# Kernel optimization log

Measured on AMD Instinct MI355X. Metric: run time of the kernel, lower is better.

Reference implementation:

```python
import jax, jax.numpy as jnp
import numpy as np

EMBED = 1024
HEADS = 16
HEAD_DIM = EMBED // HEADS
RANK = 8
ALPHA = 16.0
SCALING = ALPHA / RANK  # 2.0
B, T = 2, 2048


def setup_inputs() -> dict:
    key = jax.random.key(0)
    ks = jax.random.split(key, 12)
    d = {
        'x': jax.random.normal(ks[0], (B, T, EMBED), dtype=jnp.float32),
        'Wq': jax.random.normal(ks[1], (EMBED, EMBED), dtype=jnp.float32),
        'Aq': jax.random.normal(ks[2], (EMBED, RANK), dtype=jnp.float32) * 0.01,
        'Bq': jnp.zeros((RANK, EMBED), dtype=jnp.float32),
        'Wk': jax.random.normal(ks[3], (EMBED, EMBED), dtype=jnp.float32),
        'Ak': jax.random.normal(ks[4], (EMBED, RANK), dtype=jnp.float32) * 0.01,
        'Bk': jnp.zeros((RANK, EMBED), dtype=jnp.float32),
        'Wv': jax.random.normal(ks[5], (EMBED, EMBED), dtype=jnp.float32),
        'Av': jax.random.normal(ks[6], (EMBED, RANK), dtype=jnp.float32) * 0.01,
        'Bv': jnp.zeros((RANK, EMBED), dtype=jnp.float32),
        'Wo': jax.random.normal(ks[7], (EMBED, EMBED), dtype=jnp.float32) * (1.0 / np.sqrt(EMBED)),
        'bo': jnp.zeros((EMBED,), dtype=jnp.float32),
    }
    return d


def _lora_linear(x, W, A, Bm):
    # torch F.linear(x, W) == x @ W.T ; LoRA bypass: x @ A @ B * scaling
    base = jnp.einsum('btc,oc->bto', x, W)
    lora = (x @ A) @ Bm * SCALING
    return base + lora


def reference(x, Wq, Aq, Bq, Wk, Ak, Bk, Wv, Av, Bv, Wo, bo):
    b, t, c = x.shape
    q = _lora_linear(x, Wq, Aq, Bq).reshape(b, t, HEADS, HEAD_DIM).transpose(0, 2, 1, 3)
    k = _lora_linear(x, Wk, Ak, Bk).reshape(b, t, HEADS, HEAD_DIM).transpose(0, 2, 1, 3)
    v = _lora_linear(x, Wv, Av, Bv).reshape(b, t, HEADS, HEAD_DIM).transpose(0, 2, 1, 3)
    scores = jnp.einsum('bhqd,bhkd->bhqk', q, k) / np.sqrt(HEAD_DIM).astype(np.float32)
    attn = jax.nn.softmax(scores, axis=-1)
    ctx = jnp.einsum('bhqk,bhkd->bhqd', attn, v)  # [B,H,T,D]
    out = ctx.transpose(0, 2, 1, 3).reshape(b, t, c)
    return jnp.einsum('btc,oc->bto', out, Wo) + bo
```

## Files before the change

### kernel.cpp

```cpp
#include <hip/hip_runtime.h>
#include <hip/hip_bf16.h>
#include <math.h>

#define EMBED 1024
#define HEADS 16
#define HDIM 64
#define RANK 8
#define BB 2
#define TT 2048
#define MTOT (BB*TT)
#define BH (BB*HEADS)

typedef __attribute__((ext_vector_type(8))) short bf16x8;
typedef __attribute__((ext_vector_type(4))) float f32x4;
typedef unsigned short u16;

__device__ __forceinline__ u16 f2bf(float f){
  unsigned u = __float_as_uint(f);
  u += 0x7FFF + ((u >> 16) & 1);
  return (u16)(u >> 16);
}
__device__ __forceinline__ float bf2f(u16 h){ return __uint_as_float(((unsigned)h) << 16); }

__device__ __forceinline__ void stage16(const void* g, void* l){
  __builtin_amdgcn_global_load_lds((const __attribute__((address_space(1))) unsigned int*)g,
                                   (__attribute__((address_space(3))) unsigned int*)l, 16, 0, 0);
}

__global__ void split_x_kernel(const float* __restrict__ x, u16* __restrict__ xhi, u16* __restrict__ xlo){
  int i = blockIdx.x * 256 + threadIdx.x;
  float v = x[i];
  u16 h = f2bf(v);
  xhi[i] = h;
  xlo[i] = f2bf(v - bf2f(h));
}

__global__ void weff_split_kernel(const float* __restrict__ W, const float* __restrict__ A,
                                  const float* __restrict__ Bm,
                                  u16* __restrict__ whi, u16* __restrict__ wlo){
  int i = blockIdx.x * 256 + threadIdx.x;
  int o = i >> 10, c = i & 1023;
  float s = 0.f;
#pragma unroll
  for (int r = 0; r < RANK; ++r) s += A[c*RANK+r] * Bm[r*EMBED+o];
  float v = W[i] + 2.0f * s;
  u16 h = f2bf(v);
  whi[i] = h;
  wlo[i] = f2bf(v - bf2f(h));
}

__global__ void bf16_cast_kernel(const float* __restrict__ W, u16* __restrict__ wb){
  int i = blockIdx.x * 256 + threadIdx.x;
  wb[i] = f2bf(W[i]);
}

__device__ __forceinline__ int swz4(int row){ return (row ^ (row >> 2)) & 3; }

__global__ __launch_bounds__(256)
void qkv_gemm(const u16* __restrict__ Ahi, const u16* __restrict__ Alo,
              const u16* __restrict__ Bhi, const u16* __restrict__ Blo,
              u16* __restrict__ qhi, u16* __restrict__ qlo,
              u16* __restrict__ khi, u16* __restrict__ klo,
              u16* __restrict__ vt)
{
  __shared__ __align__(16) u16 Ah[128*32], Bh[128*32], Al[128*32], Bl[128*32];
  const int t = threadIdx.x, lane = t & 63, w = t >> 6;
  const int wr = w >> 1, wc = w & 1;
  const int fr = lane & 15, fk = lane >> 4;
  const int m0 = blockIdx.y * 128, n0 = blockIdx.x * 128;
  const bool full = (n0 < 2048);

  f32x4 acc[4][4];
#pragma unroll
  for (int i = 0; i < 4; ++i)
#pragma unroll
    for (int j = 0; j < 4; ++j) acc[i][j] = (f32x4){0.f,0.f,0.f,0.f};

  for (int k0 = 0; k0 < EMBED; k0 += 32){
    __syncthreads();
#pragma unroll
    for (int cc = 0; cc < 2; ++cc){
      int cb = w*128 + cc*64;
      int chunk = cb + lane;
      int row = chunk >> 2, slot = chunk & 3;
      int sl = slot ^ swz4(row);
      stage16(Ahi + (size_t)(m0+row)*EMBED + k0 + sl*8, Ah + cb*8);
      stage16(Bhi + (size_t)(n0+row)*EMBED + k0 + sl*8, Bh + cb*8);
      if (full){
        stage16(Alo + (size_t)(m0+row)*EMBED + k0 + sl*8, Al + cb*8);
        stage16(Blo + (size_t)(n0+row)*EMBED + k0 + sl*8, Bl + cb*8);
      }
    }
    __syncthreads();

    bf16x8 ah[4], bh[4], al[4], bl[4];
#pragma unroll
    for (int i = 0; i < 4; ++i){
      int ra = wr*64 + i*16 + fr;
      int oa = ra*32 + (fk ^ swz4(ra))*8;
      ah[i] = *(const bf16x8*)&Ah[oa];
      if (full) al[i] = *(const bf16x8*)&Al[oa];
      int rb = wc*64 + i*16 + fr;
      int ob = rb*32 + (fk ^ swz4(rb))*8;
      bh[i] = *(const bf16x8*)&Bh[ob];
      if (full) bl[i] = *(const bf16x8*)&Bl[ob];
    }
#pragma unroll
    for (int i = 0; i < 4; ++i)
#pragma unroll
      for (int j = 0; j < 4; ++j){
        acc[i][j] = __builtin_amdgcn_mfma_f32_16x16x32_bf16(ah[i], bh[j], acc[i][j], 0,0,0);
        if (full){
          acc[i][j] = __builtin_amdgcn_mfma_f32_16x16x32_bf16(ah[i], bl[j], acc[i][j], 0,0,0);
          acc[i][j] = __builtin_amdgcn_mfma_f32_16x16x32_bf16(al[i], bh[j], acc[i][j], 0,0,0);
        }
      }
  }

  const int mat = (n0 + wc*64) >> 10;
#pragma unroll
  for (int i = 0; i < 4; ++i)
#pragma unroll
    for (int j = 0; j < 4; ++j)
#pragma unroll
      for (int r = 0; r < 4; ++r){
        int gm = m0 + wr*64 + i*16 + fk*4 + r;
        int gn = n0 + wc*64 + j*16 + fr;
        int col = gn & 1023;
        float v = acc[i][j][r];
        int b = gm >> 11, tt2 = gm & 2047, h = col >> 6, d = col & 63;
        if (mat == 2){
          vt[((size_t)(b*HEADS + h)*HDIM + d)*TT + tt2] = f2bf(v);
        } else {
          if (mat == 0) v *= 0.125f;
          size_t idx = ((size_t)(b*HEADS + h)*TT + tt2)*HDIM + d;
          u16 hi = f2bf(v);
          u16 lo = f2bf(v - bf2f(hi));
          if (mat == 0){ qhi[idx] = hi; qlo[idx] = lo; }
          else         { khi[idx] = hi; klo[idx] = lo; }
        }
      }
}

__global__ __launch_bounds__(256)
void attn_mfma(const u16* __restrict__ Qhi, const u16* __restrict__ Qlo,
               const u16* __restrict__ Khi, const u16* __restrict__ Klo,
               const u16* __restrict__ Vt,  u16* __restrict__ ctx)
{
  __shared__ __align__(16) u16 smem[16384];
  u16* Kh = smem;
  u16* Kl = smem + 4096;
  u16* Vs = smem + 8192;
  u16* Ps = smem + 12288;
  const int t = threadIdx.x, lane = t & 63, w = t >> 6;
  const int fr = lane & 15, fk = lane >> 4;
  const int bh = blockIdx.y, q0 = blockIdx.x * 64;
  const size_t kbase = (size_t)bh * TT * HDIM;
  const size_t vbase = (size_t)bh * HDIM * TT;

#pragma unroll
  for (int cc = 0; cc < 2; ++cc){
    int cb = w*128 + cc*64;
    int chunk = cb + lane;
    int row = chunk >> 3, slot = chunk & 7;
    int sl = slot ^ (row & 7);
    stage16(Qhi + kbase + (size_t)(q0+row)*HDIM + sl*8, Kh + cb*8);
    stage16(Qlo + kbase + (size_t)(q0+row)*HDIM + sl*8, Kl + cb*8);
  }
  __syncthreads();
  bf16x8 qh[2], ql[2];
#pragma unroll
  for (int ks = 0; ks < 2; ++ks){
    int row = w*16 + fr;
    int off = row*64 + ((ks*4 + fk) ^ (row & 7))*8;
    qh[ks] = *(const bf16x8*)&Kh[off];
    ql[ks] = *(const bf16x8*)&Kl[off];
  }

  float mi[4], li[4];
  f32x4 oacc[4];
#pragma unroll
  for (int r = 0; r < 4; ++r){ mi[r] = -1e30f; li[r] = 0.f; }
#pragma unroll
  for (int n = 0; n < 4; ++n) oacc[n] = (f32x4){0.f,0.f,0.f,0.f};

  for (int kt = 0; kt < TT/64; ++kt){
    int kv0 = kt * 64;
    __syncthreads();
#pragma unroll
    for (int cc = 0; cc < 2; ++cc){
      int cb = w*128 + cc*64;
      int chunk = cb + lane;
      int row = chunk >> 3, slot = chunk & 7;
      int sl = slot ^ (row & 7);
      stage16(Khi + kbase + (size_t)(kv0+row)*HDIM + sl*8, Kh + cb*8);
      stage16(Klo + kbase + (size_t)(kv0+row)*HDIM + sl*8, Kl + cb*8);
      stage16(Vt  + vbase + (size_t)row*TT + kv0 + sl*8,  Vs + cb*8);
    }
    __syncthreads();

    f32x4 sacc[4];
#pragma unroll
    for (int n = 0; n < 4; ++n) sacc[n] = (f32x4){0.f,0.f,0.f,0.f};
#pragma unroll
    for (int n = 0; n < 4; ++n)
#pragma unroll
      for (int ks = 0; ks < 2; ++ks){
        int row = n*16 + fr;
        int off = row*64 + ((ks*4 + fk) ^ (row & 7))*8;
        bf16x8 kh = *(const bf16x8*)&Kh[off];
        bf16x8 kl = *(const bf16x8*)&Kl[off];
        sacc[n] = __builtin_amdgcn_mfma_f32_16x16x32_bf16(qh[ks], kh, sacc[n], 0,0,0);
        sacc[n] = __builtin_amdgcn_mfma_f32_16x16x32_bf16(qh[ks], kl, sacc[n], 0,0,0);
        sacc[n] = __builtin_amdgcn_mfma_f32_16x16x32_bf16(ql[ks], kh, sacc[n], 0,0,0);
      }

    float mt[4];
#pragma unroll
    for (int r = 0; r < 4; ++r){
      float m = fmaxf(fmaxf(sacc[0][r], sacc[1][r]), fmaxf(sacc[2][r], sacc[3][r]));
#pragma unroll
      for (int off = 1; off < 16; off <<= 1) m = fmaxf(m, __shfl_xor(m, off));
      mt[r] = m;
    }
    bool dfr = true;
#pragma unroll
    for (int r = 0; r < 4; ++r) dfr = dfr && (mt[r] - mi[r] <= 8.0f);
    if (!__all(dfr)){
#pragma unroll
      for (int r = 0; r < 4; ++r){
        float mn = fmaxf(mi[r], mt[r]);
        float sc = __expf(mi[r] - mn);
        mi[r] = mn;
        li[r] *= sc;
#pragma unroll
        for (int n = 0; n < 4; ++n) oacc[n][r] *= sc;
      }
    }
    float rsum[4] = {0.f,0.f,0.f,0.f};
#pragma unroll
    for (int n = 0; n < 4; ++n)
#pragma unroll
      for (int r = 0; r < 4; ++r){
        float p = __expf(sacc[n][r] - mi[r]);
        sacc[n][r] = p;
        rsum[r] += p;
      }
#pragma unroll
    for (int r = 0; r < 4; ++r){
#pragma unroll
      for (int off = 1; off < 16; off <<= 1) rsum[r] += __shfl_xor(rsum[r], off);
      li[r] += rsum[r];
    }

#pragma unroll
    for (int n = 0; n < 4; ++n)
#pragma unroll
      for (int r = 0; r < 4; ++r){
        int row = fk*4 + r;
        int col = n*16 + fr;
        int slot = col >> 3;
        Ps[w*1024 + row*64 + (slot ^ (row & 7))*8 + (col & 7)] = f2bf(sacc[n][r]);
      }

#pragma unroll
    for (int ks = 0; ks < 2; ++ks){
      bf16x8 pa = *(const bf16x8*)&Ps[w*1024 + fr*64 + ((ks*4 + fk) ^ (fr & 7))*8];
#pragma unroll
      for (int n = 0; n < 4; ++n){
        int row = n*16 + fr;
        bf16x8 bv = *(const bf16x8*)&Vs[row*64 + ((ks*4 + fk) ^ (row & 7))*8];
        oacc[n] = __builtin_amdgcn_mfma_f32_16x16x32_bf16(pa, bv, oacc[n], 0,0,0);
      }
    }
  }

  int b = bh >> 4, h = bh & 15;
#pragma unroll
  for (int r = 0; r < 4; ++r){
    float inv = 1.f / li[r];
    int q = q0 + w*16 + fk*4 + r;
#pragma unroll
    for (int n = 0; n < 4; ++n){
      int d = n*16 + fr;
      ctx[((size_t)(b*TT + q))*EMBED + h*HDIM + d] = f2bf(oacc[n][r]*inv);
    }
  }
}

__global__ __launch_bounds__(256)
void outproj_gemm(const u16* __restrict__ Ab, const u16* __restrict__ Bb,
                  const float* __restrict__ bias, float* __restrict__ C)
{
  __shared__ __align__(16) u16 Ah[128*32], Bh[128*32];
  const int t = threadIdx.x, lane = t & 63, w = t >> 6;
  const int wr = w >> 1, wc = w & 1;
  const int fr = lane & 15, fk = lane >> 4;
  const int m0 = blockIdx.y * 128, n0 = blockIdx.x * 128;

  f32x4 acc[4][4];
#pragma unroll
  for (int i = 0; i < 4; ++i)
#pragma unroll
    for (int j = 0; j < 4; ++j) acc[i][j] = (f32x4){0.f,0.f,0.f,0.f};

  for (int k0 = 0; k0 < EMBED; k0 += 32){
    __syncthreads();
#pragma unroll
    for (int cc = 0; cc < 2; ++cc){
      int cb = w*128 + cc*64;
      int chunk = cb + lane;
      int row = chunk >> 2, slot = chunk & 3;
      int sl = slot ^ swz4(row);
      stage16(Ab + (size_t)(m0+row)*EMBED + k0 + sl*8, Ah + cb*8);
      stage16(Bb + (size_t)(n0+row)*EMBED + k0 + sl*8, Bh + cb*8);
    }
    __syncthreads();

    bf16x8 ah[4], bh[4];
#pragma unroll
    for (int i = 0; i < 4; ++i){
      int ra = wr*64 + i*16 + fr;
      ah[i] = *(const bf16x8*)&Ah[ra*32 + (fk ^ swz4(ra))*8];
      int rb = wc*64 + i*16 + fr;
      bh[i] = *(const bf16x8*)&Bh[rb*32 + (fk ^ swz4(rb))*8];
    }
#pragma unroll
    for (int i = 0; i < 4; ++i)
#pragma unroll
      for (int j = 0; j < 4; ++j)
        acc[i][j] = __builtin_amdgcn_mfma_f32_16x16x32_bf16(ah[i], bh[j], acc[i][j], 0,0,0);
  }

#pragma unroll
  for (int i = 0; i < 4; ++i)
#pragma unroll
    for (int j = 0; j < 4; ++j)
#pragma unroll
      for (int r = 0; r < 4; ++r){
        int gm = m0 + wr*64 + i*16 + fk*4 + r;
        int gn = n0 + wc*64 + j*16 + fr;
        C[(size_t)gm*EMBED + gn] = acc[i][j][r] + bias[gn];
      }
}

extern "C" void kernel_launch(void* const* d_in, const int* in_sizes, int n_in,
                              void* d_out, int out_size, void* d_ws, size_t ws_size,
                              hipStream_t stream) {
  const float* x  = (const float*)d_in[0];
  const float* Wq = (const float*)d_in[1];
  const float* Aq = (const float*)d_in[2];
  const float* Bq = (const float*)d_in[3];
  const float* Wk = (const float*)d_in[4];
  const float* Ak = (const float*)d_in[5];
  const float* Bk = (const float*)d_in[6];
  const float* Wv = (const float*)d_in[7];
  const float* Av = (const float*)d_in[8];
  const float* Bv = (const float*)d_in[9];
  const float* Wo = (const float*)d_in[10];
  const float* bo = (const float*)d_in[11];
  float* out = (float*)d_out;

  char* ws = (char*)d_ws;
  const size_t MB = 1u << 20;
  u16* xhi  = (u16*)(ws + 0*MB);
  u16* xlo  = (u16*)(ws + 8*MB);
  u16* whi  = (u16*)(ws + 16*MB);
  u16* wlo  = (u16*)(ws + 22*MB);
  u16* wob  = (u16*)(ws + 28*MB);
  u16* qhi  = (u16*)(ws + 30*MB);
  u16* qlo  = (u16*)(ws + 38*MB);
  u16* khi  = (u16*)(ws + 46*MB);
  u16* klo  = (u16*)(ws + 54*MB);
  u16* vt   = (u16*)(ws + 62*MB);
  u16* ctx  = (u16*)(ws + 0*MB);

  dim3 blk(256);
  split_x_kernel<<<dim3(MTOT*EMBED/256), blk, 0, stream>>>(x, xhi, xlo);
  weff_split_kernel<<<dim3(4096), blk, 0, stream>>>(Wq, Aq, Bq, whi,           wlo);
  weff_split_kernel<<<dim3(4096), blk, 0, stream>>>(Wk, Ak, Bk, whi + 1048576, wlo + 1048576);
  weff_split_kernel<<<dim3(4096), blk, 0, stream>>>(Wv, Av, Bv, whi + 2097152, wlo + 2097152);
  bf16_cast_kernel<<<dim3(4096), blk, 0, stream>>>(Wo, wob);

  qkv_gemm<<<dim3(3*EMBED/128, MTOT/128), blk, 0, stream>>>(xhi, xlo, whi, wlo,
                                                            qhi, qlo, khi, klo, vt);

  attn_mfma<<<dim3(TT/64, BH), blk, 0, stream>>>(qhi, qlo, khi, klo, vt, ctx);

  outproj_gemm<<<dim3(EMBED/128, MTOT/128), blk, 0, stream>>>(ctx, wob, bo, out);
}
```

Before: 337.5 us.

## Transpose attention score MFMA, use exp2 softmax, pack P stores, merge prep kernels

The score MFMA now takes K as the A operand and Q as the B operand. Each lane therefore holds one query row's scores across four keys, so the row max and row sum need only two cross-lane shuffles instead of four per row. The 1/sqrt(d) scale is folded together with log2(e) into Q, so the softmax uses exp2f, and the rescale threshold moves to log2 units. P is converted with the packed bf16 instruction and written as 8-byte vector stores. The three weight-merge launches and the Wo cast are combined into one grid launch to cut launch overhead. The per-lane scale now has to be redistributed with __shfl before multiplying the O accumulators.

Measured after the change: 302.7 us. 10.3% less time.

```diff
diff --git a/kernel.cpp b/kernel.cpp
--- a/kernel.cpp
+++ b/kernel.cpp
@@ -14,6 +14,7 @@
 typedef __attribute__((ext_vector_type(8))) short bf16x8;
 typedef __attribute__((ext_vector_type(4))) float f32x4;
 typedef unsigned short u16;
+typedef unsigned int u32;
 
 __device__ __forceinline__ u16 f2bf(float f){
   unsigned u = __float_as_uint(f);
@@ -21,6 +22,12 @@
   return (u16)(u >> 16);
 }
 __device__ __forceinline__ float bf2f(u16 h){ return __uint_as_float(((unsigned)h) << 16); }
+
+__device__ __forceinline__ u32 cvtpk(float lo, float hi){
+  u32 r;
+  asm("v_cvt_pk_bf16_f32 %0, %1, %2" : "=v"(r) : "v"(lo), "v"(hi));
+  return r;
+}
 
 __device__ __forceinline__ void stage16(const void* g, void* l){
   __builtin_amdgcn_global_load_lds((const __attribute__((address_space(1))) unsigned int*)g,
@@ -35,23 +42,29 @@
   xlo[i] = f2bf(v - bf2f(h));
 }
 
-__global__ void weff_split_kernel(const float* __restrict__ W, const float* __restrict__ A,
-                                  const float* __restrict__ Bm,
-                                  u16* __restrict__ whi, u16* __restrict__ wlo){
+__global__ void prep_weights_kernel(const float* __restrict__ W0, const float* __restrict__ W1,
+                                    const float* __restrict__ W2, const float* __restrict__ W3,
+                                    const float* __restrict__ A0, const float* __restrict__ A1,
+                                    const float* __restrict__ A2,
+                                    const float* __restrict__ B0, const float* __restrict__ B1,
+                                    const float* __restrict__ B2,
+                                    u16* __restrict__ whi, u16* __restrict__ wlo,
+                                    u16* __restrict__ wob){
   int i = blockIdx.x * 256 + threadIdx.x;
+  int y = blockIdx.y;
+  if (y == 3){ wob[i] = f2bf(W3[i]); return; }
+  const float* W = (y == 0) ? W0 : (y == 1) ? W1 : W2;
+  const float* A = (y == 0) ? A0 : (y == 1) ? A1 : A2;
+  const float* Bm = (y == 0) ? B0 : (y == 1) ? B1 : B2;
   int o = i >> 10, c = i & 1023;
   float s = 0.f;
 #pragma unroll
   for (int r = 0; r < RANK; ++r) s += A[c*RANK+r] * Bm[r*EMBED+o];
   float v = W[i] + 2.0f * s;
   u16 h = f2bf(v);
-  whi[i] = h;
-  wlo[i] = f2bf(v - bf2f(h));
-}
-
-__global__ void bf16_cast_kernel(const float* __restrict__ W, u16* __restrict__ wb){
-  int i = blockIdx.x * 256 + threadIdx.x;
-  wb[i] = f2bf(W[i]);
+  size_t off = (size_t)y * 1048576 + i;
+  whi[off] = h;
+  wlo[off] = f2bf(v - bf2f(h));
 }
 
 __device__ __forceinline__ int swz4(int row){ return (row ^ (row >> 2)) & 3; }
@@ -118,6 +131,7 @@
   }
 
   const int mat = (n0 + wc*64) >> 10;
+  const float QSCALE = 0.125f * 1.44269504089f;
 #pragma unroll
   for (int i = 0; i < 4; ++i)
 #pragma unroll
@@ -132,7 +146,7 @@
         if (mat == 2){
           vt[((size_t)(b*HEADS + h)*HDIM + d)*TT + tt2] = f2bf(v);
         } else {
-          if (mat == 0) v *= 0.125f;
+          if (mat == 0) v *= QSCALE;
           size_t idx = ((size_t)(b*HEADS + h)*TT + tt2)*HDIM + d;
           u16 hi = f2bf(v);
           u16 lo = f2bf(v - bf2f(hi));
@@ -177,10 +191,8 @@
     ql[ks] = *(const bf16x8*)&Kl[off];
   }
 
-  float mi[4], li[4];
+  float mi = -1e30f, li = 0.f;
   f32x4 oacc[4];
-#pragma unroll
-  for (int r = 0; r < 4; ++r){ mi[r] = -1e30f; li[r] = 0.f; }
 #pragma unroll
   for (int n = 0; n < 4; ++n) oacc[n] = (f32x4){0.f,0.f,0.f,0.f};
 
@@ -210,58 +222,54 @@
         int off = row*64 + ((ks*4 + fk) ^ (row & 7))*8;
         bf16x8 kh = *(const bf16x8*)&Kh[off];
         bf16x8 kl = *(const bf16x8*)&Kl[off];
-        sacc[n] = __builtin_amdgcn_mfma_f32_16x16x32_bf16(qh[ks], kh, sacc[n], 0,0,0);
-        sacc[n] = __builtin_amdgcn_mfma_f32_16x16x32_bf16(qh[ks], kl, sacc[n], 0,0,0);
-        sacc[n] = __builtin_amdgcn_mfma_f32_16x16x32_bf16(ql[ks], kh, sacc[n], 0,0,0);
-      }
-
-    float mt[4];
-#pragma unroll
-    for (int r = 0; r < 4; ++r){
-      float m = fmaxf(fmaxf(sacc[0][r], sacc[1][r]), fmaxf(sacc[2][r], sacc[3][r]));
-#pragma unroll
-      for (int off = 1; off < 16; off <<= 1) m = fmaxf(m, __shfl_xor(m, off));
-      mt[r] = m;
-    }
-    bool dfr = true;
-#pragma unroll
-    for (int r = 0; r < 4; ++r) dfr = dfr && (mt[r] - mi[r] <= 8.0f);
-    if (!__all(dfr)){
+        sacc[n] = __builtin_amdgcn_mfma_f32_16x16x32_bf16(kh, qh[ks], sacc[n], 0,0,0);
+        sacc[n] = __builtin_amdgcn_mfma_f32_16x16x32_bf16(kl, qh[ks], sacc[n], 0,0,0);
+        sacc[n] = __builtin_amdgcn_mfma_f32_16x16x32_bf16(kh, ql[ks], sacc[n], 0,0,0);
+      }
+
+    float mt = fmaxf(fmaxf(sacc[0][0], sacc[0][1]), fmaxf(sacc[0][2], sacc[0][3]));
+#pragma unroll
+    for (int n = 1; n < 4; ++n)
+      mt = fmaxf(mt, fmaxf(fmaxf(sacc[n][0], sacc[n][1]), fmaxf(sacc[n][2], sacc[n][3])));
+    mt = fmaxf(mt, __shfl_xor(mt, 16));
+    mt = fmaxf(mt, __shfl_xor(mt, 32));
+
+    if (__any(mt > mi + 11.54f)){
+      float mn = fmaxf(mi, mt);
+      float sc = exp2f(mi - mn);
+      mi = mn;
+      li *= sc;
+      float sct[4];
+#pragma unroll
+      for (int r = 0; r < 4; ++r) sct[r] = __shfl(sc, fk*4 + r);
+#pragma unroll
+      for (int n = 0; n < 4; ++n)
+#pragma unroll
+        for (int r = 0; r < 4; ++r) oacc[n][r] *= sct[r];
+    }
+
+    float rs = 0.f;
+#pragma unroll
+    for (int n = 0; n < 4; ++n)
 #pragma unroll
       for (int r = 0; r < 4; ++r){
-        float mn = fmaxf(mi[r], mt[r]);
-        float sc = __expf(mi[r] - mn);
-        mi[r] = mn;
-        li[r] *= sc;
-#pragma unroll
-        for (int n = 0; n < 4; ++n) oacc[n][r] *= sc;
-      }
-    }
-    float rsum[4] = {0.f,0.f,0.f,0.f};
-#pragma unroll
-    for (int n = 0; n < 4; ++n)
-#pragma unroll
-      for (int r = 0; r < 4; ++r){
-        float p = __expf(sacc[n][r] - mi[r]);
+        float p = exp2f(sacc[n][r] - mi);
         sacc[n][r] = p;
-        rsum[r] += p;
-      }
-#pragma unroll
-    for (int r = 0; r < 4; ++r){
-#pragma unroll
-      for (int off = 1; off < 16; off <<= 1) rsum[r] += __shfl_xor(rsum[r], off);
-      li[r] += rsum[r];
-    }
-
-#pragma unroll
-    for (int n = 0; n < 4; ++n)
-#pragma unroll
-      for (int r = 0; r < 4; ++r){
-        int row = fk*4 + r;
-        int col = n*16 + fr;
-        int slot = col >> 3;
-        Ps[w*1024 + row*64 + (slot ^ (row & 7))*8 + (col & 7)] = f2bf(sacc[n][r]);
-      }
+        rs += p;
+      }
+    rs += __shfl_xor(rs, 16);
+    rs += __shfl_xor(rs, 32);
+    li += rs;
+
+#pragma unroll
+    for (int n = 0; n < 4; ++n){
+      u32 u0 = cvtpk(sacc[n][0], sacc[n][1]);
+      u32 u1 = cvtpk(sacc[n][2], sacc[n][3]);
+      int slot = n*2 + (fk >> 1);
+      int idx = w*1024 + fr*64 + (slot ^ (fr & 7))*8 + (fk & 1)*4;
+      uint2 pk; pk.x = u0; pk.y = u1;
+      *(uint2*)&Ps[idx] = pk;
+    }
 
 #pragma unroll
     for (int ks = 0; ks < 2; ++ks){
@@ -275,15 +283,19 @@
     }
   }
 
+  float inv = 1.f / li;
+  float invt[4];
+#pragma unroll
+  for (int r = 0; r < 4; ++r) invt[r] = __shfl(inv, fk*4 + r);
+
   int b = bh >> 4, h = bh & 15;
 #pragma unroll
   for (int r = 0; r < 4; ++r){
-    float inv = 1.f / li[r];
     int q = q0 + w*16 + fk*4 + r;
 #pragma unroll
     for (int n = 0; n < 4; ++n){
       int d = n*16 + fr;
-      ctx[((size_t)(b*TT + q))*EMBED + h*HDIM + d] = f2bf(oacc[n][r]*inv);
+      ctx[((size_t)(b*TT + q))*EMBED + h*HDIM + d] = f2bf(oacc[n][r]*invt[r]);
     }
   }
 }
@@ -377,10 +389,8 @@
 
   dim3 blk(256);
   split_x_kernel<<<dim3(MTOT*EMBED/256), blk, 0, stream>>>(x, xhi, xlo);
-  weff_split_kernel<<<dim3(4096), blk, 0, stream>>>(Wq, Aq, Bq, whi,           wlo);
-  weff_split_kernel<<<dim3(4096), blk, 0, stream>>>(Wk, Ak, Bk, whi + 1048576, wlo + 1048576);
-  weff_split_kernel<<<dim3(4096), blk, 0, stream>>>(Wv, Av, Bv, whi + 2097152, wlo + 2097152);
-  bf16_cast_kernel<<<dim3(4096), blk, 0, stream>>>(Wo, wob);
+  prep_weights_kernel<<<dim3(4096, 4), blk, 0, stream>>>(Wq, Wk, Wv, Wo, Aq, Ak, Av,
+                                                         Bq, Bk, Bv, whi, wlo, wob);
 
   qkv_gemm<<<dim3(3*EMBED/128, MTOT/128), blk, 0, stream>>>(xhi, xlo, whi, wlo,
                                                             qhi, qlo, khi, klo, vt);
```
